# Kernel optimization log

Hardware: AMD Instinct MI355X
Metric: run time of the kernel (lower is better)

The kernel has to match this reference:

```python
import jax, jax.numpy as jnp
import numpy as np

N_NODES = 100000
N_EDGES = 1600000
IN_DIM, HID_DIM, OUT_DIM = 128, 128, 64


def setup_inputs() -> dict:
    key = jax.random.key(0)
    ks = jax.random.split(key, 8)
    x = jax.random.normal(ks[0], (N_NODES, IN_DIM), dtype=jnp.float32)
    edge_index = jax.random.randint(ks[1], (2, N_EDGES), 0, N_NODES, dtype=jnp.int64)
    sc = 0.05
    W1 = jax.random.normal(ks[2], (IN_DIM, HID_DIM), dtype=jnp.float32) * sc
    b1 = jnp.zeros((HID_DIM,), dtype=jnp.float32)
    W2 = jax.random.normal(ks[3], (HID_DIM, HID_DIM), dtype=jnp.float32) * sc
    b2 = jnp.zeros((HID_DIM,), dtype=jnp.float32)
    W3 = jax.random.normal(ks[4], (HID_DIM, OUT_DIM), dtype=jnp.float32) * sc
    b3 = jnp.zeros((OUT_DIM,), dtype=jnp.float32)
    return {"x": x, "edge_index": edge_index, "W1": W1, "b1": b1,
            "W2": W2, "b2": b2, "W3": W3, "b3": b3}


def _gcn_conv(x, src, dst, norm, W, b, n_nodes):
    # x' = D^{-1/2} (A + I) D^{-1/2} (x W) + b   (PyG GCNConv default)
    h = x @ W                                   # [N, F_out]
    msg = h[src] * norm[:, None]                # gather + scale, [E+N, F_out]
    agg = jax.ops.segment_sum(msg, dst, num_segments=n_nodes)  # scatter-add
    return agg + b


def _build_norm(edge_index, n_nodes):
    # add self-loops, compute symmetric normalization coefficients
    loops = jnp.arange(n_nodes, dtype=edge_index.dtype)
    src = jnp.concatenate([edge_index[0], loops])
    dst = jnp.concatenate([edge_index[1], loops])
    deg = jax.ops.segment_sum(jnp.ones_like(dst, dtype=jnp.float32), dst,
                              num_segments=n_nodes)
    dinv = jnp.where(deg > 0, jax.lax.rsqrt(jnp.maximum(deg, 1.0)), 0.0)
    norm = dinv[src] * dinv[dst]
    return src, dst, norm


def reference(x, edge_index, W1, b1, W2, b2, W3, b3):
    n = x.shape[0]
    src, dst, norm = _build_norm(edge_index, n)
    h = jax.nn.relu(_gcn_conv(x, src, dst, norm, W1, b1, n))
    h = jax.nn.relu(_gcn_conv(h, src, dst, norm, W2, b2, n))
    out = _gcn_conv(h, src, dst, norm, W3, b3, n)
    return out
```

## Files before the change

kernel.cpp:

```cpp
#include <hip/hip_runtime.h>
#include <hip/hip_fp16.h>
#include <cstdint>
#include <cstddef>
#include <type_traits>

#define NN 100000
#define NE 1600000
#define SCAN_BLOCKS ((NN + 1023) / 1024)
#define NBK ((NN + 255) / 256)
#define BCAP 4608
#define EPB 4096
#define BIN_BLOCKS ((NE + EPB - 1) / EPB)

using half8 = __attribute__((ext_vector_type(8))) _Float16;
using f32x4 = __attribute__((ext_vector_type(4))) float;

union F4H8 { float4 f4; __half2 h2[4]; };

__device__ __forceinline__ uint2 pack4half(float4 v) {
    __half2 a = __floats2half2_rn(v.x, v.y);
    __half2 b = __floats2half2_rn(v.z, v.w);
    uint2 r;
    r.x = *(unsigned int*)&a;
    r.y = *(unsigned int*)&b;
    return r;
}

__global__ void detect_flag_kernel(const int* __restrict__ idx, int* __restrict__ flag) {
    __shared__ int cnt;
    if (threadIdx.x == 0) cnt = 0;
    __syncthreads();
    if (idx[2 * threadIdx.x + 1] == 0) atomicAdd(&cnt, 1);
    __syncthreads();
    if (threadIdx.x == 0) *flag = (cnt == (int)blockDim.x) ? 1 : 0;
}

__global__ __launch_bounds__(256) void bin_kernel(const void* __restrict__ idx,
                                                  const int* __restrict__ flag,
                                                  int* __restrict__ gcnt,
                                                  int* __restrict__ bucketbuf) {
    __shared__ int cnt[NBK];
    __shared__ int gbase[NBK];
    int t = threadIdx.x;
    long long base = (long long)blockIdx.x * EPB;
    for (int i = t; i < NBK; i += 256) cnt[i] = 0;
    __syncthreads();
    bool is64 = (*flag != 0);
    int lpos[16], d16[16], s16[16];
#pragma unroll
    for (int j = 0; j < 16; j++) {
        long long e = base + j * 256 + t;
        lpos[j] = 0; d16[j] = 0; s16[j] = 0;
        if (e < NE) {
            int s_, d_;
            if (is64) { const long long* p = (const long long*)idx; s_ = (int)p[e]; d_ = (int)p[NE + e]; }
            else      { const int* p = (const int*)idx;             s_ = p[e];      d_ = p[NE + e]; }
            d16[j] = d_; s16[j] = s_;
            lpos[j] = atomicAdd(&cnt[d_ >> 8], 1);
        }
    }
    __syncthreads();
    for (int b = t; b < NBK; b += 256) {
        int c = cnt[b];
        gbase[b] = (c > 0) ? atomicAdd(&gcnt[b * 16], c) : 0;
    }
    __syncthreads();
#pragma unroll
    for (int j = 0; j < 16; j++) {
        long long e = base + j * 256 + t;
        if (e < NE) {
            int b = d16[j] >> 8;
            int pos = gbase[b] + lpos[j];
            if (pos < BCAP) bucketbuf[(size_t)b * BCAP + pos] = (s16[j] << 8) | (d16[j] & 255);
        }
    }
}

__global__ __launch_bounds__(256) void hist_kernel(const int* __restrict__ gcnt,
                                                   const int* __restrict__ bucketbuf,
                                                   int* __restrict__ deg,
                                                   float* __restrict__ dinv) {
    __shared__ int cnt[256];
    int t = threadIdx.x, b = blockIdx.x;
    cnt[t] = 0;
    __syncthreads();
    int n = gcnt[b * 16]; if (n > BCAP) n = BCAP;
    for (int i = t; i < n; i += 256)
        atomicAdd(&cnt[bucketbuf[(size_t)b * BCAP + i] & 255], 1);
    __syncthreads();
    int node = b * 256 + t;
    if (node < NN) {
        int d = cnt[t];
        deg[node] = d;
        dinv[node] = rsqrtf((float)(d + 1));
    }
}

__global__ __launch_bounds__(256) void scanA_kernel(const int* __restrict__ deg,
                                                    int* __restrict__ blocksum) {
    __shared__ int red[256];
    int t = threadIdx.x;
    int base = blockIdx.x * 1024 + t * 4;
    int s = 0;
#pragma unroll
    for (int j = 0; j < 4; j++) { int i = base + j; if (i < NN) s += deg[i]; }
    red[t] = s;
    __syncthreads();
    for (int off = 128; off > 0; off >>= 1) {
        if (t < off) red[t] += red[t + off];
        __syncthreads();
    }
    if (t == 0) blocksum[blockIdx.x] = red[0];
}

__global__ __launch_bounds__(256) void scanC_kernel(const int* __restrict__ deg,
                                                    const int* __restrict__ blocksum,
                                                    int* __restrict__ row_start) {
    __shared__ int lds[256];
    __shared__ int boff_s;
    int t = threadIdx.x;
    int b = blockIdx.x;
    lds[t] = (t < b && t < SCAN_BLOCKS) ? blocksum[t] : 0;
    __syncthreads();
    for (int off = 128; off > 0; off >>= 1) {
        if (t < off) lds[t] += lds[t + off];
        __syncthreads();
    }
    if (t == 0) boff_s = lds[0];
    __syncthreads();
    int boff = boff_s;

    int base = b * 1024 + t * 4;
    int d[4]; int s = 0;
#pragma unroll
    for (int j = 0; j < 4; j++) { int i = base + j; d[j] = (i < NN) ? deg[i] : 0; s += d[j]; }
    __syncthreads();
    lds[t] = s;
    __syncthreads();
    for (int off = 1; off < 256; off <<= 1) {
        int u = (t >= off) ? lds[t - off] : 0;
        __syncthreads();
        lds[t] += u;
        __syncthreads();
    }
    int offr = boff + ((t == 0) ? 0 : lds[t - 1]);
#pragma unroll
    for (int j = 0; j < 4; j++) {
        int i = base + j;
        if (i < NN) { row_start[i] = offr; offr += d[j]; }
    }
    if (b == 0 && t == 0) row_start[NN] = NE;
}

__global__ __launch_bounds__(256) void csrfill_kernel(const int* __restrict__ gcnt,
                                                      const int* __restrict__ bucketbuf,
                                                      const int* __restrict__ row_start,
                                                      int* __restrict__ csr) {
    __shared__ int cur[256];
    int t = threadIdx.x, b = blockIdx.x;
    int node = b * 256 + t;
    cur[t] = (node < NN) ? row_start[node] : 0;
    __syncthreads();
    int n = gcnt[b * 16]; if (n > BCAP) n = BCAP;
    for (int i = t; i < n; i += 256) {
        int v = bucketbuf[(size_t)b * BCAP + i];
        int pos = atomicAdd(&cur[v & 255], 1);
        csr[pos] = v >> 8;
    }
}

__global__ void wt_kernel(const float* __restrict__ W, __half* __restrict__ Wt, int F) {
    int i = blockIdx.x * 256 + threadIdx.x;
    if (i >= 128 * F) return;
    int k = i / F, n = i % F;
    Wt[(size_t)n * 128 + k] = __float2half(W[i]);
}

template <int F, typename AT>
__global__ __launch_bounds__(256) void mfma_gemm_kernel(const AT* __restrict__ A,
                                                        const __half* __restrict__ Wt,
                                                        const float* __restrict__ dinv,
                                                        __half* __restrict__ H, int N) {
    constexpr int K = 128;
    constexpr int NT = F / 16;
    constexpr int FP = F + 8;
    __shared__ __half hs[64 * FP];

    int wave = threadIdx.x >> 6;
    int lane = threadIdx.x & 63;
    int quad = lane >> 4;
    int l16  = lane & 15;
    int rowbase = blockIdx.x * 64 + wave * 16;
    int arow = rowbase + l16; if (arow >= N) arow = N - 1;

    half8 afrag[4];
    const AT* ap = A + (size_t)arow * K + quad * 8;
#pragma unroll
    for (int s = 0; s < 4; s++) {
        if constexpr (std::is_same<AT, float>::value) {
            float4 u0 = *(const float4*)(ap + s * 32);
            float4 u1 = *(const float4*)(ap + s * 32 + 4);
            half8 h;
            h[0] = (_Float16)u0.x; h[1] = (_Float16)u0.y;
            h[2] = (_Float16)u0.z; h[3] = (_Float16)u0.w;
            h[4] = (_Float16)u1.x; h[5] = (_Float16)u1.y;
            h[6] = (_Float16)u1.z; h[7] = (_Float16)u1.w;
            afrag[s] = h;
        } else {
            afrag[s] = *(const half8*)(ap + s * 32);
        }
    }

    f32x4 acc[NT];
#pragma unroll
    for (int t = 0; t < NT; t++) acc[t] = (f32x4){0.f, 0.f, 0.f, 0.f};

#pragma unroll
    for (int s = 0; s < 4; s++) {
#pragma unroll
        for (int t = 0; t < NT; t++) {
            half8 b = *(const half8*)(Wt + (size_t)(t * 16 + l16) * K + s * 32 + quad * 8);
            acc[t] = __builtin_amdgcn_mfma_f32_16x16x32_f16(afrag[s], b, acc[t], 0, 0, 0);
        }
    }

    float dv[4];
#pragma unroll
    for (int r = 0; r < 4; r++) {
        int grow = rowbase + quad * 4 + r;
        dv[r] = (grow < N) ? dinv[grow] : 0.f;
    }
#pragma unroll
    for (int t = 0; t < NT; t++) {
#pragma unroll
        for (int r = 0; r < 4; r++) {
            int lrow = wave * 16 + quad * 4 + r;
            hs[lrow * FP + t * 16 + l16] = __float2half(acc[t][r] * dv[r]);
        }
    }
    __syncthreads();
    constexpr int CHUNKS = 64 * F / 8;
    for (int i = threadIdx.x; i < CHUNKS; i += 256) {
        int row = i / (F / 8);
        int col8 = (i % (F / 8)) * 8;
        int grow = blockIdx.x * 64 + row;
        if (grow < N)
            *(uint4*)&H[(size_t)grow * F + col8] = *(const uint4*)&hs[row * FP + col8];
    }
}

template <int FO>
__global__ __launch_bounds__(256) void agg_gemm_kernel(const __half* __restrict__ Hs,
                                                       const int* __restrict__ rs,
                                                       const int* __restrict__ csr,
                                                       const float* __restrict__ dinv,
                                                       const float* __restrict__ bias,
                                                       const __half* __restrict__ Wt,
                                                       __half* __restrict__ Hout) {
    constexpr int FI = 128;
    constexpr int FP = FI + 8;
    constexpr int FPO = FO + 8;
    constexpr int NT4 = FO / 64;
    __shared__ __half Alds[16 * FP];

    int tid = threadIdx.x;
    int nodebase = blockIdx.x * 16;
    int lrow = tid / 16;
    int node = nodebase + lrow;
    int q = (tid % 16) * 8;

    float dn = dinv[node];
    float acc[8];
    {
        F4H8 u; u.f4 = *(const float4*)&Hs[(size_t)node * FI + q];
#pragma unroll
        for (int j = 0; j < 4; j++) {
            float2 f = __half22float2(u.h2[j]);
            acc[2 * j] = f.x; acc[2 * j + 1] = f.y;
        }
    }
    int e = rs[node];
    int e1 = rs[node + 1];
    for (; e + 8 <= e1; e += 8) {
        int s[8];
#pragma unroll
        for (int j = 0; j < 8; j++) s[j] = csr[e + j];
        F4H8 h[8];
#pragma unroll
        for (int j = 0; j < 8; j++) h[j].f4 = *(const float4*)&Hs[(size_t)s[j] * FI + q];
#pragma unroll
        for (int j = 0; j < 8; j++) {
#pragma unroll
            for (int k = 0; k < 4; k++) {
                float2 f = __half22float2(h[j].h2[k]);
                acc[2 * k] += f.x; acc[2 * k + 1] += f.y;
            }
        }
    }
    for (; e < e1; e++) {
        int s = csr[e];
        F4H8 u; u.f4 = *(const float4*)&Hs[(size_t)s * FI + q];
#pragma unroll
        for (int k = 0; k < 4; k++) {
            float2 f = __half22float2(u.h2[k]);
            acc[2 * k] += f.x; acc[2 * k + 1] += f.y;
        }
    }
    float4 b0 = *(const float4*)&bias[q];
    float4 b1 = *(const float4*)&bias[q + 4];
    float o[8];
    o[0] = fmaxf(dn * acc[0] + b0.x, 0.f); o[1] = fmaxf(dn * acc[1] + b0.y, 0.f);
    o[2] = fmaxf(dn * acc[2] + b0.z, 0.f); o[3] = fmaxf(dn * acc[3] + b0.w, 0.f);
    o[4] = fmaxf(dn * acc[4] + b1.x, 0.f); o[5] = fmaxf(dn * acc[5] + b1.y, 0.f);
    o[6] = fmaxf(dn * acc[6] + b1.z, 0.f); o[7] = fmaxf(dn * acc[7] + b1.w, 0.f);
    {
        uint4 p;
        uint2 a = pack4half(make_float4(o[0], o[1], o[2], o[3]));
        uint2 b = pack4half(make_float4(o[4], o[5], o[6], o[7]));
        p.x = a.x; p.y = a.y; p.z = b.x; p.w = b.y;
        *(uint4*)&Alds[lrow * FP + q] = p;
    }
    __syncthreads();

    int wave = tid >> 6;
    int lane = tid & 63;
    int quad = lane >> 4;
    int l16  = lane & 15;

    half8 afrag[4];
#pragma unroll
    for (int s = 0; s < 4; s++)
        afrag[s] = *(const half8*)&Alds[l16 * FP + s * 32 + quad * 8];

    f32x4 cacc[NT4];
#pragma unroll
    for (int t = 0; t < NT4; t++) cacc[t] = (f32x4){0.f, 0.f, 0.f, 0.f};
#pragma unroll
    for (int s = 0; s < 4; s++) {
#pragma unroll
        for (int t = 0; t < NT4; t++) {
            int tile = wave * NT4 + t;
            half8 b = *(const half8*)(Wt + (size_t)(tile * 16 + l16) * FI + s * 32 + quad * 8);
            cacc[t] = __builtin_amdgcn_mfma_f32_16x16x32_f16(afrag[s], b, cacc[t], 0, 0, 0);
        }
    }
    __syncthreads();

    float dv[4];
#pragma unroll
    for (int r = 0; r < 4; r++) dv[r] = dinv[nodebase + quad * 4 + r];
#pragma unroll
    for (int t = 0; t < NT4; t++) {
        int colb = (wave * NT4 + t) * 16 + l16;
#pragma unroll
        for (int r = 0; r < 4; r++)
            Alds[(quad * 4 + r) * FPO + colb] = __float2half(cacc[t][r] * dv[r]);
    }
    __syncthreads();
    constexpr int CHUNKS = 16 * FO / 8;
    for (int i = tid; i < CHUNKS; i += 256) {
        int row = i / (FO / 8);
        int col8 = (i % (FO / 8)) * 8;
        *(uint4*)&Hout[(size_t)(nodebase + row) * FO + col8] = *(const uint4*)&Alds[row * FPO + col8];
    }
}

template <int F>
__global__ __launch_bounds__(256) void agg_kernel(const __half* __restrict__ Hs,
                                                  const int* __restrict__ rs,
                                                  const int* __restrict__ csr,
                                                  const float* __restrict__ dinv,
                                                  const float* __restrict__ bias,
                                                  float* __restrict__ OUT) {
    constexpr int CQ = F / 8;
    constexpr int NPB = 256 / CQ;
    int node = blockIdx.x * NPB + threadIdx.x / CQ;
    int q = (threadIdx.x % CQ) * 8;
    if (node >= NN) return;
    float dn = dinv[node];
    float acc[8];
    {
        F4H8 u; u.f4 = *(const float4*)&Hs[(size_t)node * F + q];
#pragma unroll
        for (int j = 0; j < 4; j++) {
            float2 f = __half22float2(u.h2[j]);
            acc[2 * j] = f.x; acc[2 * j + 1] = f.y;
        }
    }
    int e = rs[node];
    int e1 = rs[node + 1];
    for (; e + 8 <= e1; e += 8) {
        int s[8];
#pragma unroll
        for (int j = 0; j < 8; j++) s[j] = csr[e + j];
        F4H8 h[8];
#pragma unroll
        for (int j = 0; j < 8; j++) h[j].f4 = *(const float4*)&Hs[(size_t)s[j] * F + q];
#pragma unroll
        for (int j = 0; j < 8; j++) {
#pragma unroll
            for (int k = 0; k < 4; k++) {
                float2 f = __half22float2(h[j].h2[k]);
                acc[2 * k] += f.x; acc[2 * k + 1] += f.y;
            }
        }
    }
    for (; e < e1; e++) {
        int s = csr[e];
        F4H8 u; u.f4 = *(const float4*)&Hs[(size_t)s * F + q];
#pragma unroll
        for (int k = 0; k < 4; k++) {
            float2 f = __half22float2(u.h2[k]);
            acc[2 * k] += f.x; acc[2 * k + 1] += f.y;
        }
    }
    float4 o0 = make_float4(dn * acc[0] + bias[q],     dn * acc[1] + bias[q + 1],
                            dn * acc[2] + bias[q + 2], dn * acc[3] + bias[q + 3]);
    float4 o1 = make_float4(dn * acc[4] + bias[q + 4], dn * acc[5] + bias[q + 5],
                            dn * acc[6] + bias[q + 6], dn * acc[7] + bias[q + 7]);
    *(float4*)&OUT[(size_t)node * F + q]     = o0;
    *(float4*)&OUT[(size_t)node * F + q + 4] = o1;
}

extern "C" void kernel_launch(void* const* d_in, const int* in_sizes, int n_in,
                              void* d_out, int out_size, void* d_ws, size_t ws_size,
                              hipStream_t stream) {
    const float* x  = (const float*)d_in[0];
    const void* eidx = d_in[1];
    const float* W1 = (const float*)d_in[2];
    const float* b1 = (const float*)d_in[3];
    const float* W2 = (const float*)d_in[4];
    const float* b2 = (const float*)d_in[5];
    const float* W3 = (const float*)d_in[6];
    const float* b3 = (const float*)d_in[7];
    float* out = (float*)d_out;

    char* ws = (char*)d_ws;
    size_t off = 0;
    auto alloc = [&](size_t bytes) -> void* {
        void* p = ws + off;
        off += (bytes + 255) & ~(size_t)255;
        return p;
    };
    __half* bufA = (__half*)alloc((size_t)NN * 128 * 2);
    int* bucketbuf = (int*)bufA;
    int* gcnt      = (int*)((char*)bufA + (size_t)NBK * BCAP * 4);
    __half* bufC = (__half*)alloc((size_t)NN * 128 * 2);
    int* deg      = (int*)bufC;
    int* blocksum = (int*)((char*)bufC + (size_t)NN * 4);
    int* row_start = (int*)alloc((size_t)(NN + 1) * 4);
    float* dinv = (float*)alloc((size_t)NN * 4);
    int* flagp  = (int*)alloc(256);
    int* csr    = (int*)alloc((size_t)NE * 4);
    __half* Wt1 = (__half*)alloc((size_t)128 * 128 * 2);
    __half* Wt2 = (__half*)alloc((size_t)128 * 128 * 2);
    __half* Wt3 = (__half*)alloc((size_t)64 * 128 * 2);

    hipMemsetAsync(gcnt, 0, (size_t)NBK * 16 * 4, stream);
    detect_flag_kernel<<<1, 256, 0, stream>>>((const int*)eidx, flagp);
    bin_kernel<<<BIN_BLOCKS, 256, 0, stream>>>(eidx, flagp, gcnt, bucketbuf);
    hist_kernel<<<NBK, 256, 0, stream>>>(gcnt, bucketbuf, deg, dinv);
    scanA_kernel<<<SCAN_BLOCKS, 256, 0, stream>>>(deg, blocksum);
    scanC_kernel<<<SCAN_BLOCKS, 256, 0, stream>>>(deg, blocksum, row_start);
    csrfill_kernel<<<NBK, 256, 0, stream>>>(gcnt, bucketbuf, row_start, csr);

    wt_kernel<<<(128 * 128 + 255) / 256, 256, 0, stream>>>(W1, Wt1, 128);
    wt_kernel<<<(128 * 128 + 255) / 256, 256, 0, stream>>>(W2, Wt2, 128);
    wt_kernel<<<(128 * 64 + 255) / 256, 256, 0, stream>>>(W3, Wt3, 64);

    const int GB = (NN + 63) / 64;
    mfma_gemm_kernel<128, float><<<GB, 256, 0, stream>>>(x, Wt1, dinv, bufA, NN);
    agg_gemm_kernel<128><<<NN / 16, 256, 0, stream>>>(bufA, row_start, csr, dinv, b1, Wt2, bufC);
    agg_gemm_kernel<64><<<NN / 16, 256, 0, stream>>>(bufC, row_start, csr, dinv, b2, Wt3, bufA);
    agg_kernel<64><<<NN / 32, 256, 0, stream>>>(bufA, row_start, csr, dinv, b3, out);
}
```

Before: 378.1 us.

## Use column-chunked feature layout and split aggregation from GEMM

Feature matrices are stored as 16-column slabs of shape [F/16][N][16], so each gather reads one contiguous 32-byte piece per source node within a slab. The fused aggregate+GEMM kernels are split into a slab-wise aggregation kernel, one thread per node per chunk, and a separate column-major GEMM kernel. The aim is a smaller gather working set per block, which should raise cache hit rates during the random neighbour gathers. Nontemporal loads and stores are added for the CSR indices and outputs. The cost is extra kernel launches and an extra round trip of intermediate features through global memory.

```diff
diff --git a/kernel.cpp b/kernel.cpp
--- a/kernel.cpp
+++ b/kernel.cpp
@@ -14,6 +14,7 @@
 
 using half8 = __attribute__((ext_vector_type(8))) _Float16;
 using f32x4 = __attribute__((ext_vector_type(4))) float;
+using u32x4 = __attribute__((ext_vector_type(4))) unsigned int;
 
 union F4H8 { float4 f4; __half2 h2[4]; };
 
@@ -24,6 +25,15 @@
     r.x = *(unsigned int*)&a;
     r.y = *(unsigned int*)&b;
     return r;
+}
+
+__device__ __forceinline__ void acc8(float* acc, const F4H8& u) {
+#pragma unroll
+    for (int k = 0; k < 4; k++) {
+        float2 f = __half22float2(u.h2[k]);
+        acc[2 * k] += f.x;
+        acc[2 * k + 1] += f.y;
+    }
 }
 
 __global__ void detect_flag_kernel(const int* __restrict__ idx, int* __restrict__ flag) {
@@ -239,187 +249,228 @@
         }
     }
     __syncthreads();
-    constexpr int CHUNKS = 64 * F / 8;
-    for (int i = threadIdx.x; i < CHUNKS; i += 256) {
-        int row = i / (F / 8);
-        int col8 = (i % (F / 8)) * 8;
+    for (int i = threadIdx.x; i < NT * 64; i += 256) {
+        int c = i >> 6;
+        int row = i & 63;
         int grow = blockIdx.x * 64 + row;
-        if (grow < N)
-            *(uint4*)&H[(size_t)grow * F + col8] = *(const uint4*)&hs[row * FP + col8];
+        if (grow < N) {
+            __half* dst = H + ((size_t)c * NN + grow) * 16;
+            const __half* srcp = &hs[row * FP + c * 16];
+            __builtin_nontemporal_store(*(const u32x4*)srcp, (u32x4*)dst);
+            __builtin_nontemporal_store(*(const u32x4*)(srcp + 8), (u32x4*)(dst + 8));
+        }
     }
 }
 
 template <int FO>
-__global__ __launch_bounds__(256) void agg_gemm_kernel(const __half* __restrict__ Hs,
-                                                       const int* __restrict__ rs,
-                                                       const int* __restrict__ csr,
-                                                       const float* __restrict__ dinv,
-                                                       const float* __restrict__ bias,
-                                                       const __half* __restrict__ Wt,
-                                                       __half* __restrict__ Hout) {
-    constexpr int FI = 128;
-    constexpr int FP = FI + 8;
-    constexpr int FPO = FO + 8;
-    constexpr int NT4 = FO / 64;
-    __shared__ __half Alds[16 * FP];
-
-    int tid = threadIdx.x;
-    int nodebase = blockIdx.x * 16;
-    int lrow = tid / 16;
-    int node = nodebase + lrow;
-    int q = (tid % 16) * 8;
+__global__ __launch_bounds__(256) void gemm_cm_kernel(const __half* __restrict__ A,
+                                                      const __half* __restrict__ Wt,
+                                                      const float* __restrict__ dinv,
+                                                      __half* __restrict__ H, int N) {
+    constexpr int K = 128;
+    constexpr int NT = FO / 16;
+    constexpr int FP = FO + 8;
+    __shared__ __half hs[64 * FP];
+
+    int wave = threadIdx.x >> 6;
+    int lane = threadIdx.x & 63;
+    int quad = lane >> 4;
+    int l16  = lane & 15;
+    int rowbase = blockIdx.x * 64 + wave * 16;
+    int arow = rowbase + l16; if (arow >= N) arow = N - 1;
+
+    half8 afrag[4];
+#pragma unroll
+    for (int s = 0; s < 4; s++) {
+        int f0 = s * 32 + quad * 8;
+        afrag[s] = *(const half8*)(A + ((size_t)(f0 >> 4) * NN + arow) * 16 + (f0 & 8));
+    }
+
+    f32x4 acc[NT];
+#pragma unroll
+    for (int t = 0; t < NT; t++) acc[t] = (f32x4){0.f, 0.f, 0.f, 0.f};
+
+#pragma unroll
+    for (int s = 0; s < 4; s++) {
+#pragma unroll
+        for (int t = 0; t < NT; t++) {
+            half8 b = *(const half8*)(Wt + (size_t)(t * 16 + l16) * K + s * 32 + quad * 8);
+            acc[t] = __builtin_amdgcn_mfma_f32_16x16x32_f16(afrag[s], b, acc[t], 0, 0, 0);
+        }
+    }
+
+    float dv[4];
+#pragma unroll
+    for (int r = 0; r < 4; r++) {
+        int grow = rowbase + quad * 4 + r;
+        dv[r] = (grow < N) ? dinv[grow] : 0.f;
+    }
+#pragma unroll
+    for (int t = 0; t < NT; t++) {
+#pragma unroll
+        for (int r = 0; r < 4; r++) {
+            int lrow = wave * 16 + quad * 4 + r;
+            hs[lrow * FP + t * 16 + l16] = __float2half(acc[t][r] * dv[r]);
+        }
+    }
+    __syncthreads();
+    for (int i = threadIdx.x; i < NT * 64; i += 256) {
+        int c = i >> 6;
+        int row = i & 63;
+        int grow = blockIdx.x * 64 + row;
+        if (grow < N) {
+            __half* dst = H + ((size_t)c * NN + grow) * 16;
+            const __half* srcp = &hs[row * FP + c * 16];
+            __builtin_nontemporal_store(*(const u32x4*)srcp, (u32x4*)dst);
+            __builtin_nontemporal_store(*(const u32x4*)(srcp + 8), (u32x4*)(dst + 8));
+        }
+    }
+}
+
+__global__ __launch_bounds__(256) void agg_h_kernel(const __half* __restrict__ Hs,
+                                                    const int* __restrict__ rs,
+                                                    const int* __restrict__ csr,
+                                                    const float* __restrict__ dinv,
+                                                    const float* __restrict__ bias,
+                                                    __half* __restrict__ Out) {
+    int chunk = blockIdx.x & 7;
+    int nb = blockIdx.x >> 3;
+    int node = nb * 256 + threadIdx.x;
+    if (node >= NN) return;
+    const __half* slab = Hs + (size_t)chunk * ((size_t)NN * 16);
+
+    float acc[16];
+    {
+        F4H8 u0, u1;
+        u0.f4 = *(const float4*)(slab + (size_t)node * 16);
+        u1.f4 = *(const float4*)(slab + (size_t)node * 16 + 8);
+#pragma unroll
+        for (int k = 0; k < 4; k++) {
+            float2 f0 = __half22float2(u0.h2[k]);
+            float2 f1 = __half22float2(u1.h2[k]);
+            acc[2 * k] = f0.x;     acc[2 * k + 1] = f0.y;
+            acc[8 + 2 * k] = f1.x; acc[8 + 2 * k + 1] = f1.y;
+        }
+    }
+    int e  = __builtin_nontemporal_load(&rs[node]);
+    int e1 = __builtin_nontemporal_load(&rs[node + 1]);
+    for (; e + 4 <= e1; e += 4) {
+        int s0 = __builtin_nontemporal_load(&csr[e]);
+        int s1 = __builtin_nontemporal_load(&csr[e + 1]);
+        int s2 = __builtin_nontemporal_load(&csr[e + 2]);
+        int s3 = __builtin_nontemporal_load(&csr[e + 3]);
+        F4H8 a0, b0, a1, b1, a2, b2, a3, b3;
+        a0.f4 = *(const float4*)(slab + (size_t)s0 * 16);
+        b0.f4 = *(const float4*)(slab + (size_t)s0 * 16 + 8);
+        a1.f4 = *(const float4*)(slab + (size_t)s1 * 16);
+        b1.f4 = *(const float4*)(slab + (size_t)s1 * 16 + 8);
+        a2.f4 = *(const float4*)(slab + (size_t)s2 * 16);
+        b2.f4 = *(const float4*)(slab + (size_t)s2 * 16 + 8);
+        a3.f4 = *(const float4*)(slab + (size_t)s3 * 16);
+        b3.f4 = *(const float4*)(slab + (size_t)s3 * 16 + 8);
+        acc8(acc, a0); acc8(acc + 8, b0);
+        acc8(acc, a1); acc8(acc + 8, b1);
+        acc8(acc, a2); acc8(acc + 8, b2);
+        acc8(acc, a3); acc8(acc + 8, b3);
+    }
+    for (; e < e1; e++) {
+        int s = __builtin_nontemporal_load(&csr[e]);
+        F4H8 u0, u1;
+        u0.f4 = *(const float4*)(slab + (size_t)s * 16);
+        u1.f4 = *(const float4*)(slab + (size_t)s * 16 + 8);
+        acc8(acc, u0); acc8(acc + 8, u1);
+    }
 
     float dn = dinv[node];
-    float acc[8];
+    const float* bp = bias + chunk * 16;
+    float o[16];
+#pragma unroll
+    for (int j = 0; j < 16; j++) o[j] = fmaxf(fmaf(dn, acc[j], bp[j]), 0.f);
+
+    u32x4 p0, p1;
     {
-        F4H8 u; u.f4 = *(const float4*)&Hs[(size_t)node * FI + q];
-#pragma unroll
-        for (int j = 0; j < 4; j++) {
-            float2 f = __half22float2(u.h2[j]);
-            acc[2 * j] = f.x; acc[2 * j + 1] = f.y;
-        }
-    }
-    int e = rs[node];
-    int e1 = rs[node + 1];
-    for (; e + 8 <= e1; e += 8) {
-        int s[8];
-#pragma unroll
-        for (int j = 0; j < 8; j++) s[j] = csr[e + j];
-        F4H8 h[8];
-#pragma unroll
-        for (int j = 0; j < 8; j++) h[j].f4 = *(const float4*)&Hs[(size_t)s[j] * FI + q];
-#pragma unroll
-        for (int j = 0; j < 8; j++) {
-#pragma unroll
-            for (int k = 0; k < 4; k++) {
-                float2 f = __half22float2(h[j].h2[k]);
-                acc[2 * k] += f.x; acc[2 * k + 1] += f.y;
-            }
-        }
-    }
-    for (; e < e1; e++) {
-        int s = csr[e];
-        F4H8 u; u.f4 = *(const float4*)&Hs[(size_t)s * FI + q];
-#pragma unroll
-        for (int k = 0; k < 4; k++) {
-            float2 f = __half22float2(u.h2[k]);
-            acc[2 * k] += f.x; acc[2 * k + 1] += f.y;
-        }
-    }
-    float4 b0 = *(const float4*)&bias[q];
-    float4 b1 = *(const float4*)&bias[q + 4];
-    float o[8];
-    o[0] = fmaxf(dn * acc[0] + b0.x, 0.f); o[1] = fmaxf(dn * acc[1] + b0.y, 0.f);
-    o[2] = fmaxf(dn * acc[2] + b0.z, 0.f); o[3] = fmaxf(dn * acc[3] + b0.w, 0.f);
-    o[4] = fmaxf(dn * acc[4] + b1.x, 0.f); o[5] = fmaxf(dn * acc[5] + b1.y, 0.f);
-    o[6] = fmaxf(dn * acc[6] + b1.z, 0.f); o[7] = fmaxf(dn * acc[7] + b1.w, 0.f);
-    {
-        uint4 p;
         uint2 a = pack4half(make_float4(o[0], o[1], o[2], o[3]));
         uint2 b = pack4half(make_float4(o[4], o[5], o[6], o[7]));
-        p.x = a.x; p.y = a.y; p.z = b.x; p.w = b.y;
-        *(uint4*)&Alds[lrow * FP + q] = p;
-    }
-    __syncthreads();
-
-    int wave = tid >> 6;
-    int lane = tid & 63;
-    int quad = lane >> 4;
-    int l16  = lane & 15;
-
-    half8 afrag[4];
-#pragma unroll
-    for (int s = 0; s < 4; s++)
-        afrag[s] = *(const half8*)&Alds[l16 * FP + s * 32 + quad * 8];
-
-    f32x4 cacc[NT4];
-#pragma unroll
-    for (int t = 0; t < NT4; t++) cacc[t] = (f32x4){0.f, 0.f, 0.f, 0.f};
-#pragma unroll
-    for (int s = 0; s < 4; s++) {
-#pragma unroll
-        for (int t = 0; t < NT4; t++) {
-            int tile = wave * NT4 + t;
-            half8 b = *(const half8*)(Wt + (size_t)(tile * 16 + l16) * FI + s * 32 + quad * 8);
-            cacc[t] = __builtin_amdgcn_mfma_f32_16x16x32_f16(afrag[s], b, cacc[t], 0, 0, 0);
-        }
-    }
-    __syncthreads();
-
-    float dv[4];
-#pragma unroll
-    for (int r = 0; r < 4; r++) dv[r] = dinv[nodebase + quad * 4 + r];
-#pragma unroll
-    for (int t = 0; t < NT4; t++) {
-        int colb = (wave * NT4 + t) * 16 + l16;
-#pragma unroll
-        for (int r = 0; r < 4; r++)
-            Alds[(quad * 4 + r) * FPO + colb] = __float2half(cacc[t][r] * dv[r]);
-    }
-    __syncthreads();
-    constexpr int CHUNKS = 16 * FO / 8;
-    for (int i = tid; i < CHUNKS; i += 256) {
-        int row = i / (FO / 8);
-        int col8 = (i % (FO / 8)) * 8;
-        *(uint4*)&Hout[(size_t)(nodebase + row) * FO + col8] = *(const uint4*)&Alds[row * FPO + col8];
-    }
-}
-
-template <int F>
-__global__ __launch_bounds__(256) void agg_kernel(const __half* __restrict__ Hs,
-                                                  const int* __restrict__ rs,
-                                                  const int* __restrict__ csr,
-                                                  const float* __restrict__ dinv,
-                                                  const float* __restrict__ bias,
-                                                  float* __restrict__ OUT) {
-    constexpr int CQ = F / 8;
-    constexpr int NPB = 256 / CQ;
-    int node = blockIdx.x * NPB + threadIdx.x / CQ;
-    int q = (threadIdx.x % CQ) * 8;
+        p0[0] = a.x; p0[1] = a.y; p0[2] = b.x; p0[3] = b.y;
+        uint2 c = pack4half(make_float4(o[8], o[9], o[10], o[11]));
+        uint2 d = pack4half(make_float4(o[12], o[13], o[14], o[15]));
+        p1[0] = c.x; p1[1] = c.y; p1[2] = d.x; p1[3] = d.y;
+    }
+    __half* op = Out + (size_t)chunk * ((size_t)NN * 16) + (size_t)node * 16;
+    __builtin_nontemporal_store(p0, (u32x4*)op);
+    __builtin_nontemporal_store(p1, (u32x4*)(op + 8));
+}
+
+__global__ __launch_bounds__(256) void agg_out_kernel(const __half* __restrict__ Hs,
+                                                      const int* __restrict__ rs,
+                                                      const int* __restrict__ csr,
+                                                      const float* __restrict__ dinv,
+                                                      const float* __restrict__ bias,
+                                                      float* __restrict__ OUT) {
+    int l = blockIdx.x & 7;
+    int chunk = l >> 1;
+    int nb = (blockIdx.x >> 3) * 2 + (l & 1);
+    int node = nb * 256 + threadIdx.x;
     if (node >= NN) return;
+    const __half* slab = Hs + (size_t)chunk * ((size_t)NN * 16);
+
+    float acc[16];
+    {
+        F4H8 u0, u1;
+        u0.f4 = *(const float4*)(slab + (size_t)node * 16);
+        u1.f4 = *(const float4*)(slab + (size_t)node * 16 + 8);
+#pragma unroll
+        for (int k = 0; k < 4; k++) {
+            float2 f0 = __half22float2(u0.h2[k]);
+            float2 f1 = __half22float2(u1.h2[k]);
+            acc[2 * k] = f0.x;     acc[2 * k + 1] = f0.y;
+            acc[8 + 2 * k] = f1.x; acc[8 + 2 * k + 1] = f1.y;
+        }
+    }
+    int e  = __builtin_nontemporal_load(&rs[node]);
+    int e1 = __builtin_nontemporal_load(&rs[node + 1]);
+    for (; e + 4 <= e1; e += 4) {
+        int s0 = __builtin_nontemporal_load(&csr[e]);
+        int s1 = __builtin_nontemporal_load(&csr[e + 1]);
+        int s2 = __builtin_nontemporal_load(&csr[e + 2]);
+        int s3 = __builtin_nontemporal_load(&csr[e + 3]);
+        F4H8 a0, b0, a1, b1, a2, b2, a3, b3;
+        a0.f4 = *(const float4*)(slab + (size_t)s0 * 16);
+        b0.f4 = *(const float4*)(slab + (size_t)s0 * 16 + 8);
+        a1.f4 = *(const float4*)(slab + (size_t)s1 * 16);
+        b1.f4 = *(const float4*)(slab + (size_t)s1 * 16 + 8);
+        a2.f4 = *(const float4*)(slab + (size_t)s2 * 16);
+        b2.f4 = *(const float4*)(slab + (size_t)s2 * 16 + 8);
+        a3.f4 = *(const float4*)(slab + (size_t)s3 * 16);
+        b3.f4 = *(const float4*)(slab + (size_t)s3 * 16 + 8);
+        acc8(acc, a0); acc8(acc + 8, b0);
+        acc8(acc, a1); acc8(acc + 8, b1);
+        acc8(acc, a2); acc8(acc + 8, b2);
+        acc8(acc, a3); acc8(acc + 8, b3);
+    }
+    for (; e < e1; e++) {
+        int s = __builtin_nontemporal_load(&csr[e]);
+        F4H8 u0, u1;
+        u0.f4 = *(const float4*)(slab + (size_t)s * 16);
+        u1.f4 = *(const float4*)(slab + (size_t)s * 16 + 8);
+        acc8(acc, u0); acc8(acc + 8, u1);
+    }
+
     float dn = dinv[node];
-    float acc[8];
-    {
-        F4H8 u; u.f4 = *(const float4*)&Hs[(size_t)node * F + q];
-#pragma unroll
-        for (int j = 0; j < 4; j++) {
-            float2 f = __half22float2(u.h2[j]);
-            acc[2 * j] = f.x; acc[2 * j + 1] = f.y;
-        }
-    }
-    int e = rs[node];
-    int e1 = rs[node + 1];
-    for (; e + 8 <= e1; e += 8) {
-        int s[8];
-#pragma unroll
-        for (int j = 0; j < 8; j++) s[j] = csr[e + j];
-        F4H8 h[8];
-#pragma unroll
-        for (int j = 0; j < 8; j++) h[j].f4 = *(const float4*)&Hs[(size_t)s[j] * F + q];
-#pragma unroll
-        for (int j = 0; j < 8; j++) {
-#pragma unroll
-            for (int k = 0; k < 4; k++) {
-                float2 f = __half22float2(h[j].h2[k]);
-                acc[2 * k] += f.x; acc[2 * k + 1] += f.y;
-            }
-        }
-    }
-    for (; e < e1; e++) {
-        int s = csr[e];
-        F4H8 u; u.f4 = *(const float4*)&Hs[(size_t)s * F + q];
-#pragma unroll
-        for (int k = 0; k < 4; k++) {
-            float2 f = __half22float2(u.h2[k]);
-            acc[2 * k] += f.x; acc[2 * k + 1] += f.y;
-        }
-    }
-    float4 o0 = make_float4(dn * acc[0] + bias[q],     dn * acc[1] + bias[q + 1],
-                            dn * acc[2] + bias[q + 2], dn * acc[3] + bias[q + 3]);
-    float4 o1 = make_float4(dn * acc[4] + bias[q + 4], dn * acc[5] + bias[q + 5],
-                            dn * acc[6] + bias[q + 6], dn * acc[7] + bias[q + 7]);
-    *(float4*)&OUT[(size_t)node * F + q]     = o0;
-    *(float4*)&OUT[(size_t)node * F + q + 4] = o1;
+    const float* bp = bias + chunk * 16;
+    float o[16];
+#pragma unroll
+    for (int j = 0; j < 16; j++) o[j] = fmaf(dn, acc[j], bp[j]);
+
+    float* op = OUT + (size_t)node * 64 + chunk * 16;
+    f32x4 v0 = {o[0], o[1], o[2], o[3]};
+    f32x4 v1 = {o[4], o[5], o[6], o[7]};
+    f32x4 v2 = {o[8], o[9], o[10], o[11]};
+    f32x4 v3 = {o[12], o[13], o[14], o[15]};
+    __builtin_nontemporal_store(v0, (f32x4*)op);
+    __builtin_nontemporal_store(v1, (f32x4*)(op + 4));
+    __builtin_nontemporal_store(v2, (f32x4*)(op + 8));
+    __builtin_nontemporal_store(v3, (f32x4*)(op + 12));
 }
 
 extern "C" void kernel_launch(void* const* d_in, const int* in_sizes, int n_in,
@@ -470,7 +521,9 @@
 
     const int GB = (NN + 63) / 64;
     mfma_gemm_kernel<128, float><<<GB, 256, 0, stream>>>(x, Wt1, dinv, bufA, NN);
-    agg_gemm_kernel<128><<<NN / 16, 256, 0, stream>>>(bufA, row_start, csr, dinv, b1, Wt2, bufC);
-    agg_gemm_kernel<64><<<NN / 16, 256, 0, stream>>>(bufC, row_start, csr, dinv, b2, Wt3, bufA);
-    agg_kernel<64><<<NN / 32, 256, 0, stream>>>(bufA, row_start, csr, dinv, b3, out);
-}
+    agg_h_kernel<<<NBK * 8, 256, 0, stream>>>(bufA, row_start, csr, dinv, b1, bufC);
+    gemm_cm_kernel<128><<<GB, 256, 0, stream>>>(bufC, Wt2, dinv, bufA, NN);
+    agg_h_kernel<<<NBK * 8, 256, 0, stream>>>(bufA, row_start, csr, dinv, b2, bufC);
+    gemm_cm_kernel<64><<<GB, 256, 0, stream>>>(bufC, Wt3, dinv, bufA, NN);
+    agg_out_kernel<<<((NBK + 1) / 2) * 8, 256, 0, stream>>>(bufA, row_start, csr, dinv, b3, out);
+}
```

Result: slower. 621.4 us (+64.3%).

## Split fused aggregation+GEMM into separate aggregation and MFMA GEMM kernels

Applied to the files above, without the earlier changes.

Replaces the fused per-layer kernel, which aggregated neighbours into LDS and then ran a 16-row MFMA GEMM, with a plain aggregation kernel writing fp16 features followed by the existing tiled MFMA GEMM kernel. The aggregation kernel loses its LDS staging and barriers, which may raise occupancy for the latency-bound gather, and the GEMM runs with 64-row tiles. In exchange, an extra intermediate feature matrix is written and reread per layer, and two more kernel launches are added.

```diff
diff --git a/kernel.cpp b/kernel.cpp
--- a/kernel.cpp
+++ b/kernel.cpp
@@ -24,6 +24,15 @@
     r.x = *(unsigned int*)&a;
     r.y = *(unsigned int*)&b;
     return r;
+}
+
+__device__ __forceinline__ void acc8(float* acc, const F4H8& u) {
+#pragma unroll
+    for (int k = 0; k < 4; k++) {
+        float2 f = __half22float2(u.h2[k]);
+        acc[2 * k] += f.x;
+        acc[2 * k + 1] += f.y;
+    }
 }
 
 __global__ void detect_flag_kernel(const int* __restrict__ idx, int* __restrict__ flag) {
@@ -249,30 +258,22 @@
     }
 }
 
-template <int FO>
-__global__ __launch_bounds__(256) void agg_gemm_kernel(const __half* __restrict__ Hs,
-                                                       const int* __restrict__ rs,
-                                                       const int* __restrict__ csr,
-                                                       const float* __restrict__ dinv,
-                                                       const float* __restrict__ bias,
-                                                       const __half* __restrict__ Wt,
-                                                       __half* __restrict__ Hout) {
-    constexpr int FI = 128;
-    constexpr int FP = FI + 8;
-    constexpr int FPO = FO + 8;
-    constexpr int NT4 = FO / 64;
-    __shared__ __half Alds[16 * FP];
-
-    int tid = threadIdx.x;
-    int nodebase = blockIdx.x * 16;
-    int lrow = tid / 16;
-    int node = nodebase + lrow;
-    int q = (tid % 16) * 8;
-
+template <int F>
+__global__ __launch_bounds__(256) void agg_h16_kernel(const __half* __restrict__ Hs,
+                                                      const int* __restrict__ rs,
+                                                      const int* __restrict__ csr,
+                                                      const float* __restrict__ dinv,
+                                                      const float* __restrict__ bias,
+                                                      __half* __restrict__ H) {
+    constexpr int CQ = F / 8;
+    constexpr int NPB = 256 / CQ;
+    int node = blockIdx.x * NPB + threadIdx.x / CQ;
+    int q = (threadIdx.x % CQ) * 8;
+    if (node >= NN) return;
     float dn = dinv[node];
     float acc[8];
     {
-        F4H8 u; u.f4 = *(const float4*)&Hs[(size_t)node * FI + q];
+        F4H8 u; u.f4 = *(const float4*)&Hs[(size_t)node * F + q];
 #pragma unroll
         for (int j = 0; j < 4; j++) {
             float2 f = __half22float2(u.h2[j]);
@@ -287,24 +288,14 @@
         for (int j = 0; j < 8; j++) s[j] = csr[e + j];
         F4H8 h[8];
 #pragma unroll
-        for (int j = 0; j < 8; j++) h[j].f4 = *(const float4*)&Hs[(size_t)s[j] * FI + q];
-#pragma unroll
-        for (int j = 0; j < 8; j++) {
-#pragma unroll
-            for (int k = 0; k < 4; k++) {
-                float2 f = __half22float2(h[j].h2[k]);
-                acc[2 * k] += f.x; acc[2 * k + 1] += f.y;
-            }
-        }
+        for (int j = 0; j < 8; j++) h[j].f4 = *(const float4*)&Hs[(size_t)s[j] * F + q];
+#pragma unroll
+        for (int j = 0; j < 8; j++) acc8(acc, h[j]);
     }
     for (; e < e1; e++) {
         int s = csr[e];
-        F4H8 u; u.f4 = *(const float4*)&Hs[(size_t)s * FI + q];
-#pragma unroll
-        for (int k = 0; k < 4; k++) {
-            float2 f = __half22float2(u.h2[k]);
-            acc[2 * k] += f.x; acc[2 * k + 1] += f.y;
-        }
+        F4H8 u; u.f4 = *(const float4*)&Hs[(size_t)s * F + q];
+        acc8(acc, u);
     }
     float4 b0 = *(const float4*)&bias[q];
     float4 b1 = *(const float4*)&bias[q + 4];
@@ -313,56 +304,11 @@
     o[2] = fmaxf(dn * acc[2] + b0.z, 0.f); o[3] = fmaxf(dn * acc[3] + b0.w, 0.f);
     o[4] = fmaxf(dn * acc[4] + b1.x, 0.f); o[5] = fmaxf(dn * acc[5] + b1.y, 0.f);
     o[6] = fmaxf(dn * acc[6] + b1.z, 0.f); o[7] = fmaxf(dn * acc[7] + b1.w, 0.f);
-    {
-        uint4 p;
-        uint2 a = pack4half(make_float4(o[0], o[1], o[2], o[3]));
-        uint2 b = pack4half(make_float4(o[4], o[5], o[6], o[7]));
-        p.x = a.x; p.y = a.y; p.z = b.x; p.w = b.y;
-        *(uint4*)&Alds[lrow * FP + q] = p;
-    }
-    __syncthreads();
-
-    int wave = tid >> 6;
-    int lane = tid & 63;
-    int quad = lane >> 4;
-    int l16  = lane & 15;
-
-    half8 afrag[4];
-#pragma unroll
-    for (int s = 0; s < 4; s++)
-        afrag[s] = *(const half8*)&Alds[l16 * FP + s * 32 + quad * 8];
-
-    f32x4 cacc[NT4];
-#pragma unroll
-    for (int t = 0; t < NT4; t++) cacc[t] = (f32x4){0.f, 0.f, 0.f, 0.f};
-#pragma unroll
-    for (int s = 0; s < 4; s++) {
-#pragma unroll
-        for (int t = 0; t < NT4; t++) {
-            int tile = wave * NT4 + t;
-            half8 b = *(const half8*)(Wt + (size_t)(tile * 16 + l16) * FI + s * 32 + quad * 8);
-            cacc[t] = __builtin_amdgcn_mfma_f32_16x16x32_f16(afrag[s], b, cacc[t], 0, 0, 0);
-        }
-    }
-    __syncthreads();
-
-    float dv[4];
-#pragma unroll
-    for (int r = 0; r < 4; r++) dv[r] = dinv[nodebase + quad * 4 + r];
-#pragma unroll
-    for (int t = 0; t < NT4; t++) {
-        int colb = (wave * NT4 + t) * 16 + l16;
-#pragma unroll
-        for (int r = 0; r < 4; r++)
-            Alds[(quad * 4 + r) * FPO + colb] = __float2half(cacc[t][r] * dv[r]);
-    }
-    __syncthreads();
-    constexpr int CHUNKS = 16 * FO / 8;
-    for (int i = tid; i < CHUNKS; i += 256) {
-        int row = i / (FO / 8);
-        int col8 = (i % (FO / 8)) * 8;
-        *(uint4*)&Hout[(size_t)(nodebase + row) * FO + col8] = *(const uint4*)&Alds[row * FPO + col8];
-    }
+    uint4 p;
+    uint2 a = pack4half(make_float4(o[0], o[1], o[2], o[3]));
+    uint2 b = pack4half(make_float4(o[4], o[5], o[6], o[7]));
+    p.x = a.x; p.y = a.y; p.z = b.x; p.w = b.y;
+    *(uint4*)&H[(size_t)node * F + q] = p;
 }
 
 template <int F>
@@ -397,22 +343,12 @@
 #pragma unroll
         for (int j = 0; j < 8; j++) h[j].f4 = *(const float4*)&Hs[(size_t)s[j] * F + q];
 #pragma unroll
-        for (int j = 0; j < 8; j++) {
-#pragma unroll
-            for (int k = 0; k < 4; k++) {
-                float2 f = __half22float2(h[j].h2[k]);
-                acc[2 * k] += f.x; acc[2 * k + 1] += f.y;
-            }
-        }
+        for (int j = 0; j < 8; j++) acc8(acc, h[j]);
     }
     for (; e < e1; e++) {
         int s = csr[e];
         F4H8 u; u.f4 = *(const float4*)&Hs[(size_t)s * F + q];
-#pragma unroll
-        for (int k = 0; k < 4; k++) {
-            float2 f = __half22float2(u.h2[k]);
-            acc[2 * k] += f.x; acc[2 * k + 1] += f.y;
-        }
+        acc8(acc, u);
     }
     float4 o0 = make_float4(dn * acc[0] + bias[q],     dn * acc[1] + bias[q + 1],
                             dn * acc[2] + bias[q + 2], dn * acc[3] + bias[q + 3]);
@@ -470,7 +406,9 @@
 
     const int GB = (NN + 63) / 64;
     mfma_gemm_kernel<128, float><<<GB, 256, 0, stream>>>(x, Wt1, dinv, bufA, NN);
-    agg_gemm_kernel<128><<<NN / 16, 256, 0, stream>>>(bufA, row_start, csr, dinv, b1, Wt2, bufC);
-    agg_gemm_kernel<64><<<NN / 16, 256, 0, stream>>>(bufC, row_start, csr, dinv, b2, Wt3, bufA);
+    agg_h16_kernel<128><<<NN / 16, 256, 0, stream>>>(bufA, row_start, csr, dinv, b1, bufC);
+    mfma_gemm_kernel<128, __half><<<GB, 256, 0, stream>>>(bufC, Wt2, dinv, bufA, NN);
+    agg_h16_kernel<128><<<NN / 16, 256, 0, stream>>>(bufA, row_start, csr, dinv, b2, bufC);
+    mfma_gemm_kernel<64, __half><<<GB, 256, 0, stream>>>(bufC, Wt3, dinv, bufA, NN);
     agg_kernel<64><<<NN / 32, 256, 0, stream>>>(bufA, row_start, csr, dinv, b3, out);
 }
```

Result: slower. 407.4 us (+7.7%).

## Process nodes in degree-sorted order to balance aggregation workloads

Applied to the files above, without the earlier changes.

Adds a counting sort of nodes by in-degree (histogram, scan, scatter) that builds a permutation. The aggregation kernels then walk nodes through that permutation, so each block and wavefront handles nodes of similar degree and loses less time to divergent loop lengths. The cost is three extra small kernels plus scattered output writes and less locality in the per-node reads.

```diff
diff --git a/kernel.cpp b/kernel.cpp
--- a/kernel.cpp
+++ b/kernel.cpp
@@ -24,6 +24,15 @@
     r.x = *(unsigned int*)&a;
     r.y = *(unsigned int*)&b;
     return r;
+}
+
+__device__ __forceinline__ void acc8(float* acc, const F4H8& u) {
+#pragma unroll
+    for (int k = 0; k < 4; k++) {
+        float2 f = __half22float2(u.h2[k]);
+        acc[2 * k] += f.x;
+        acc[2 * k + 1] += f.y;
+    }
 }
 
 __global__ void detect_flag_kernel(const int* __restrict__ idx, int* __restrict__ flag) {
@@ -167,6 +176,55 @@
         int pos = atomicAdd(&cur[v & 255], 1);
         csr[pos] = v >> 8;
     }
+}
+
+__global__ __launch_bounds__(256) void dhist_kernel(const int* __restrict__ deg,
+                                                    int* __restrict__ dbins) {
+    __shared__ int h[256];
+    int t = threadIdx.x;
+    h[t] = 0;
+    __syncthreads();
+    int i = blockIdx.x * 256 + t;
+    if (i < NN) {
+        int d = deg[i]; if (d > 255) d = 255;
+        atomicAdd(&h[d], 1);
+    }
+    __syncthreads();
+    if (h[t] > 0) atomicAdd(&dbins[t], h[t]);
+}
+
+__global__ void dscan_kernel(const int* __restrict__ dbins, int* __restrict__ dstart) {
+    __shared__ int lds[256];
+    int t = threadIdx.x;
+    lds[t] = dbins[t];
+    __syncthreads();
+    if (t == 0) {
+        int s = 0;
+        for (int i = 0; i < 256; i++) { int v = lds[i]; lds[i] = s; s += v; }
+    }
+    __syncthreads();
+    dstart[t] = lds[t];
+}
+
+__global__ __launch_bounds__(256) void dscatter_kernel(const int* __restrict__ deg,
+                                                       int* __restrict__ dstart,
+                                                       int* __restrict__ perm) {
+    __shared__ int h[256];
+    __shared__ int base[256];
+    int t = threadIdx.x;
+    h[t] = 0;
+    __syncthreads();
+    int i = blockIdx.x * 256 + t;
+    int d = 0, lpos = 0;
+    bool valid = (i < NN);
+    if (valid) {
+        d = deg[i]; if (d > 255) d = 255;
+        lpos = atomicAdd(&h[d], 1);
+    }
+    __syncthreads();
+    base[t] = (h[t] > 0) ? atomicAdd(&dstart[t], h[t]) : 0;
+    __syncthreads();
+    if (valid) perm[base[d] + lpos] = i;
 }
 
 __global__ void wt_kernel(const float* __restrict__ W, __half* __restrict__ Wt, int F) {
@@ -256,17 +314,21 @@
                                                        const float* __restrict__ dinv,
                                                        const float* __restrict__ bias,
                                                        const __half* __restrict__ Wt,
+                                                       const int* __restrict__ perm,
                                                        __half* __restrict__ Hout) {
     constexpr int FI = 128;
     constexpr int FP = FI + 8;
     constexpr int FPO = FO + 8;
     constexpr int NT4 = FO / 64;
     __shared__ __half Alds[16 * FP];
+    __shared__ int nids[16];
 
     int tid = threadIdx.x;
     int nodebase = blockIdx.x * 16;
+    if (tid < 16) nids[tid] = perm[nodebase + tid];
+    __syncthreads();
     int lrow = tid / 16;
-    int node = nodebase + lrow;
+    int node = nids[lrow];
     int q = (tid % 16) * 8;
 
     float dn = dinv[node];
@@ -289,22 +351,12 @@
 #pragma unroll
         for (int j = 0; j < 8; j++) h[j].f4 = *(const float4*)&Hs[(size_t)s[j] * FI + q];
 #pragma unroll
-        for (int j = 0; j < 8; j++) {
-#pragma unroll
-            for (int k = 0; k < 4; k++) {
-                float2 f = __half22float2(h[j].h2[k]);
-                acc[2 * k] += f.x; acc[2 * k + 1] += f.y;
-            }
-        }
+        for (int j = 0; j < 8; j++) acc8(acc, h[j]);
     }
     for (; e < e1; e++) {
         int s = csr[e];
         F4H8 u; u.f4 = *(const float4*)&Hs[(size_t)s * FI + q];
-#pragma unroll
-        for (int k = 0; k < 4; k++) {
-            float2 f = __half22float2(u.h2[k]);
-            acc[2 * k] += f.x; acc[2 * k + 1] += f.y;
-        }
+        acc8(acc, u);
     }
     float4 b0 = *(const float4*)&bias[q];
     float4 b1 = *(const float4*)&bias[q + 4];
@@ -348,7 +400,7 @@
 
     float dv[4];
 #pragma unroll
-    for (int r = 0; r < 4; r++) dv[r] = dinv[nodebase + quad * 4 + r];
+    for (int r = 0; r < 4; r++) dv[r] = dinv[nids[quad * 4 + r]];
 #pragma unroll
     for (int t = 0; t < NT4; t++) {
         int colb = (wave * NT4 + t) * 16 + l16;
@@ -361,7 +413,7 @@
     for (int i = tid; i < CHUNKS; i += 256) {
         int row = i / (FO / 8);
         int col8 = (i % (FO / 8)) * 8;
-        *(uint4*)&Hout[(size_t)(nodebase + row) * FO + col8] = *(const uint4*)&Alds[row * FPO + col8];
+        *(uint4*)&Hout[(size_t)nids[row] * FO + col8] = *(const uint4*)&Alds[row * FPO + col8];
     }
 }
 
@@ -371,12 +423,14 @@
                                                   const int* __restrict__ csr,
                                                   const float* __restrict__ dinv,
                                                   const float* __restrict__ bias,
+                                                  const int* __restrict__ perm,
                                                   float* __restrict__ OUT) {
     constexpr int CQ = F / 8;
     constexpr int NPB = 256 / CQ;
-    int node = blockIdx.x * NPB + threadIdx.x / CQ;
+    int pidx = blockIdx.x * NPB + threadIdx.x / CQ;
+    if (pidx >= NN) return;
+    int node = perm[pidx];
     int q = (threadIdx.x % CQ) * 8;
-    if (node >= NN) return;
     float dn = dinv[node];
     float acc[8];
     {
@@ -397,22 +451,12 @@
 #pragma unroll
         for (int j = 0; j < 8; j++) h[j].f4 = *(const float4*)&Hs[(size_t)s[j] * F + q];
 #pragma unroll
-        for (int j = 0; j < 8; j++) {
-#pragma unroll
-            for (int k = 0; k < 4; k++) {
-                float2 f = __half22float2(h[j].h2[k]);
-                acc[2 * k] += f.x; acc[2 * k + 1] += f.y;
-            }
-        }
+        for (int j = 0; j < 8; j++) acc8(acc, h[j]);
     }
     for (; e < e1; e++) {
         int s = csr[e];
         F4H8 u; u.f4 = *(const float4*)&Hs[(size_t)s * F + q];
-#pragma unroll
-        for (int k = 0; k < 4; k++) {
-            float2 f = __half22float2(u.h2[k]);
-            acc[2 * k] += f.x; acc[2 * k + 1] += f.y;
-        }
+        acc8(acc, u);
     }
     float4 o0 = make_float4(dn * acc[0] + bias[q],     dn * acc[1] + bias[q + 1],
                             dn * acc[2] + bias[q + 2], dn * acc[3] + bias[q + 3]);
@@ -452,11 +496,15 @@
     float* dinv = (float*)alloc((size_t)NN * 4);
     int* flagp  = (int*)alloc(256);
     int* csr    = (int*)alloc((size_t)NE * 4);
+    int* perm   = (int*)alloc((size_t)NN * 4);
+    int* dbins  = (int*)alloc(256 * 4);
+    int* dstart = (int*)alloc(256 * 4);
     __half* Wt1 = (__half*)alloc((size_t)128 * 128 * 2);
     __half* Wt2 = (__half*)alloc((size_t)128 * 128 * 2);
     __half* Wt3 = (__half*)alloc((size_t)64 * 128 * 2);
 
     hipMemsetAsync(gcnt, 0, (size_t)NBK * 16 * 4, stream);
+    hipMemsetAsync(dbins, 0, 256 * 4, stream);
     detect_flag_kernel<<<1, 256, 0, stream>>>((const int*)eidx, flagp);
     bin_kernel<<<BIN_BLOCKS, 256, 0, stream>>>(eidx, flagp, gcnt, bucketbuf);
     hist_kernel<<<NBK, 256, 0, stream>>>(gcnt, bucketbuf, deg, dinv);
@@ -464,13 +512,17 @@
     scanC_kernel<<<SCAN_BLOCKS, 256, 0, stream>>>(deg, blocksum, row_start);
     csrfill_kernel<<<NBK, 256, 0, stream>>>(gcnt, bucketbuf, row_start, csr);
 
+    dhist_kernel<<<NBK, 256, 0, stream>>>(deg, dbins);
+    dscan_kernel<<<1, 256, 0, stream>>>(dbins, dstart);
+    dscatter_kernel<<<NBK, 256, 0, stream>>>(deg, dstart, perm);
+
     wt_kernel<<<(128 * 128 + 255) / 256, 256, 0, stream>>>(W1, Wt1, 128);
     wt_kernel<<<(128 * 128 + 255) / 256, 256, 0, stream>>>(W2, Wt2, 128);
     wt_kernel<<<(128 * 64 + 255) / 256, 256, 0, stream>>>(W3, Wt3, 64);
 
     const int GB = (NN + 63) / 64;
     mfma_gemm_kernel<128, float><<<GB, 256, 0, stream>>>(x, Wt1, dinv, bufA, NN);
-    agg_gemm_kernel<128><<<NN / 16, 256, 0, stream>>>(bufA, row_start, csr, dinv, b1, Wt2, bufC);
-    agg_gemm_kernel<64><<<NN / 16, 256, 0, stream>>>(bufC, row_start, csr, dinv, b2, Wt3, bufA);
-    agg_kernel<64><<<NN / 32, 256, 0, stream>>>(bufA, row_start, csr, dinv, b3, out);
-}
+    agg_gemm_kernel<128><<<NN / 16, 256, 0, stream>>>(bufA, row_start, csr, dinv, b1, Wt2, perm, bufC);
+    agg_gemm_kernel<64><<<NN / 16, 256, 0, stream>>>(bufC, row_start, csr, dinv, b2, Wt3, perm, bufA);
+    agg_kernel<64><<<NN / 32, 256, 0, stream>>>(bufA, row_start, csr, dinv, b3, perm, out);
+}
```

Measured after the change: 380.1 us. About the same (+0.5%).
